# Kernel tuning notes

Measured on AMD Instinct MI355X. Metric: run time of the kernel, lower is better.

Reference implementation:

```python
import jax, jax.numpy as jnp
import numpy as np

B, N, M, C, H = 2, 2048, 512, 1536, 12
HD = C // H          # 128 head dim
RD = 64              # partial rotary dim (rotary_dim in torch code)
EPS = 1e-6


def setup_inputs() -> dict:
    key = jax.random.key(0)
    ks = jax.random.split(key, 8)
    x = jax.random.normal(ks[0], (B, N, C), dtype=jnp.float32)
    y = jax.random.normal(ks[1], (B, M, C), dtype=jnp.float32)
    # realistic rope table: pos[n, j, 0]=cos, pos[n, j, 1]=sin, j over RD//2 freqs
    t = jnp.arange(N, dtype=jnp.float32)
    inv_freq = 1.0 / (10000.0 ** (jnp.arange(RD // 2, dtype=jnp.float32) / (RD // 2)))
    ang = t[:, None] * inv_freq[None, :]                     # [N, RD/2]
    pos = jnp.stack([jnp.cos(ang), jnp.sin(ang)], axis=-1)   # [N, RD/2, 2]
    y_token_weights = jax.random.uniform(ks[2], (B, M), dtype=jnp.float32, minval=0.05, maxval=2.0)
    s = 0.02
    Wqkv = jax.random.normal(ks[3], (C, 3 * C), dtype=jnp.float32) * s
    Wkv = jax.random.normal(ks[4], (C, 2 * C), dtype=jnp.float32) * s
    q_norm_w = jnp.ones((HD,), dtype=jnp.float32)
    k_norm_w = jnp.ones((HD,), dtype=jnp.float32)
    Wproj = jax.random.normal(ks[5], (C, C), dtype=jnp.float32) * s
    bproj = jnp.zeros((C,), dtype=jnp.float32)
    return {"x": x, "y": y, "pos": pos, "y_token_weights": y_token_weights,
            "Wqkv": Wqkv, "Wkv": Wkv, "q_norm_w": q_norm_w, "k_norm_w": k_norm_w,
            "Wproj": Wproj, "bproj": bproj}


def _rms_norm(h, w):
    # RMSNorm in fp32 then cast back (matches torch Norm)
    hf = h.astype(jnp.float32)
    var = jnp.mean(hf * hf, axis=-1, keepdims=True)
    return (w * (hf * jax.lax.rsqrt(var + EPS))).astype(h.dtype)


def _rope(q, k, pos):
    # q,k: [B,H,N,HD]; pos: [N, RD/2, 2]; rotate first RD dims only
    cos = pos[..., 0][None, None]            # [1,1,N,RD/2]
    sin = pos[..., 1][None, None]
    half = RD // 2

    def rot(t):
        t1 = t[..., :half]
        t2 = t[..., half:RD]
        t_rot = jnp.concatenate([t1 * cos - t2 * sin, t1 * sin + t2 * cos], axis=-1)
        return jnp.concatenate([t_rot, t[..., RD:]], axis=-1)

    return rot(q), rot(k)


def reference(x, y, pos, y_token_weights, Wqkv, Wkv, q_norm_w, k_norm_w, Wproj, bproj):
    # self QKV: [B,N,3C] -> [3,B,H,N,HD]
    qkv = jnp.einsum('bnc,cd->bnd', x, Wqkv).reshape(B, N, 3, H, HD).transpose(2, 0, 3, 1, 4)
    q, kx, vx = qkv[0], qkv[1], qkv[2]
    q = _rms_norm(q, q_norm_w)
    kx = _rms_norm(kx, k_norm_w)
    q, kx = _rope(q, kx, pos)

    # cross KV from y: [B,M,2C] -> [2,B,H,M,HD]
    kv = jnp.einsum('bmc,cd->bmd', y, Wkv).reshape(B, M, 2, H, HD).transpose(2, 0, 3, 1, 4)
    ky = _rms_norm(kv[0], k_norm_w)
    vy = kv[1]
    k = jnp.concatenate([kx, ky], axis=2)    # [B,H,N+M,HD]
    v = jnp.concatenate([vx, vy], axis=2)

    # additive bias: zeros over x tokens, log(clamp(w)) over y tokens
    y_bias = jnp.log(jnp.clip(y_token_weights, 1e-4, None))           # [B,M]
    attn_bias = jnp.concatenate([jnp.zeros((B, N), x.dtype), y_bias], axis=1)[:, None, None, :]

    scale = HD ** -0.5
    scores = jnp.einsum('bhnd,bhsd->bhns', q, k) * scale + attn_bias  # [B,H,N,N+M]
    attn = jax.nn.softmax(scores, axis=-1)
    out = jnp.einsum('bhns,bhsd->bhnd', attn, v)                      # [B,H,N,HD]
    out = out.transpose(0, 2, 1, 3).reshape(B, N, C)
    return jnp.einsum('bnc,cd->bnd', out, Wproj) + bproj
```

## Files before the change

kernel.cpp:

```cpp
#include <hip/hip_runtime.h>

typedef unsigned short u16;
typedef short bf16x8 __attribute__((ext_vector_type(8)));
typedef float f32x4 __attribute__((ext_vector_type(4)));
typedef u16 u16x4 __attribute__((ext_vector_type(4)));

#define DEVFN static __device__ __forceinline__

constexpr int Bz = 2, Nn = 2048, Mm = 512, Cc = 1536, Hh = 12, HD = 128;
constexpr int Ss = Nn + Mm;
constexpr float EPSV = 1e-6f;
constexpr float SCL = 0.08838834764831845f;

DEVFN u16 f2bf(float f) {
  union { float f; unsigned u; } v; v.f = f;
  unsigned r = v.u + 0x7fffu + ((v.u >> 16) & 1u);
  return (u16)(r >> 16);
}

DEVFN unsigned cvtpk(float lo, float hi) {
  unsigned r;
  asm("v_cvt_pk_bf16_f32 %0, %1, %2" : "=v"(r) : "v"(lo), "v"(hi));
  return r;
}

DEVFN void gload16(const void* g, void* l) {
  __builtin_amdgcn_global_load_lds((const __attribute__((address_space(1))) void*)g,
                                   (__attribute__((address_space(3))) void*)l, 16, 0, 0);
}

DEVFN f32x4 mfma16(bf16x8 a, bf16x8 b, f32x4 c) {
  return __builtin_amdgcn_mfma_f32_16x16x32_bf16(a, b, c, 0, 0, 0);
}


__global__ void k_convert(const float* __restrict__ in, u16* __restrict__ out, int n) {
  int i = (blockIdx.x * blockDim.x + threadIdx.x) * 4;
  if (i < n) {
    float4 v = *(const float4*)(in + i);
    u16x4 o = { f2bf(v.x), f2bf(v.y), f2bf(v.z), f2bf(v.w) };
    *(u16x4*)(out + i) = o;
  }
}

__global__ void k_transpose_conv(const float* __restrict__ in, u16* __restrict__ out,
                                 int R, int Ccols) {
  __shared__ float t[32][33];
  int c0 = blockIdx.x * 32, r0 = blockIdx.y * 32;
  int lr = threadIdx.x >> 5, lc = threadIdx.x & 31;
#pragma unroll
  for (int i = 0; i < 4; ++i)
    t[lr + 8 * i][lc] = in[(long)(r0 + lr + 8 * i) * Ccols + c0 + lc];
  __syncthreads();
#pragma unroll
  for (int i = 0; i < 4; ++i)
    out[(long)(c0 + lr + 8 * i) * R + r0 + lc] = f2bf(t[lc][lr + 8 * i]);
}

__global__ void k_bias(const float* __restrict__ w, float* __restrict__ bias) {
  int i = blockIdx.x * 256 + threadIdx.x;
  if (i < Bz * Ss) {
    int b = i / Ss, s = i % Ss;
    bias[i] = (s < Nn) ? 0.0f : logf(fmaxf(w[b * Mm + s - Nn], 1e-4f));
  }
}

template <int MODE>
__global__ __launch_bounds__(256, 2) void k_gemm(
    const u16* __restrict__ A, const u16* __restrict__ Bt,
    int K, int NC, int rowsPerB,
    const float* __restrict__ pos, const float* __restrict__ qnw,
    const float* __restrict__ knw, const float* __restrict__ bprj,
    u16* __restrict__ qout, u16* __restrict__ kout, u16* __restrict__ vout,
    float* __restrict__ fout) {
  __shared__ __align__(16) u16 As[2][128 * 64];
  __shared__ __align__(16) u16 Bs[2][128 * 64];
  __shared__ float red[256];
  const int tid = threadIdx.x;
  const int lane = tid & 63;
  const int wid = tid >> 6;
  const int g = lane >> 4, cl = lane & 15;
  const int wr = wid >> 1, wc = wid & 1;
  const long m0 = (long)blockIdx.x * 128, n0 = (long)blockIdx.y * 128;

  f32x4 acc[4][4] = {};

  const int arow0 = tid >> 3;
  const int sxb = (((tid & 7) ^ (arow0 & 7)) << 4);
  const long K2 = (long)K * 2;
  const char* Abase = (const char*)A + (m0 + arow0) * K2 + sxb;
  const char* Bbase = (const char*)Bt + (n0 + arow0) * K2 + sxb;
  const int dtid = tid * 16;

  auto STAGE = [&](int kt, int s) {
    char* ad = (char*)As[s];
    char* bd = (char*)Bs[s];
    const long ko = (long)kt * 128;
#pragma unroll
    for (int i = 0; i < 4; ++i) {
      gload16(Abase + i * 32 * K2 + ko, ad + i * 4096 + dtid);
      gload16(Bbase + i * 32 * K2 + ko, bd + i * 4096 + dtid);
    }
  };

  const int nt = K / 64;
  STAGE(0, 0);
  int cur = 0;
  for (int kt = 0; kt < nt; ++kt) {
    __syncthreads();
    if (kt + 1 < nt) STAGE(kt + 1, cur ^ 1);
    const char* as = (const char*)As[cur];
    const char* bs = (const char*)Bs[cur];
#pragma unroll
    for (int s = 0; s < 2; ++s) {
      bf16x8 af[4], bfr[4];
#pragma unroll
      for (int m = 0; m < 4; ++m) {
        int row = wr * 64 + m * 16 + cl;
        af[m] = *(const bf16x8*)(as + row * 128 + (((s * 4 + g) ^ (row & 7)) << 4));
      }
#pragma unroll
      for (int n = 0; n < 4; ++n) {
        int row = wc * 64 + n * 16 + cl;
        bfr[n] = *(const bf16x8*)(bs + row * 128 + (((s * 4 + g) ^ (row & 7)) << 4));
      }
#pragma unroll
      for (int m = 0; m < 4; ++m)
#pragma unroll
        for (int n = 0; n < 4; ++n)
          acc[m][n] = mfma16(af[m], bfr[n], acc[m][n]);
    }
    cur ^= 1;
  }

  if (MODE == 0) {
#pragma unroll
    for (int n = 0; n < 4; ++n) {
      int col = (int)n0 + wc * 64 + n * 16 + cl;
      float bv = bprj[col];
#pragma unroll
      for (int m = 0; m < 4; ++m)
#pragma unroll
        for (int r = 0; r < 4; ++r) {
          long row = m0 + wr * 64 + m * 16 + 4 * g + r;
          fout[row * NC + col] = acc[m][n][r] + bv;
        }
    }
    return;
  }

  const int ct = blockIdx.y;
  const int s_idx = ct / Hh, h = ct % Hh;
  const int bb = (int)(m0 / rowsPerB);
  const int bh = bb * Hh + h;
  const int seq0 = (int)(m0 % rowsPerB) + wr * 64;
  const bool is_v = (MODE == 1) ? (s_idx == 2) : (s_idx == 1);
  const bool do_norm = !is_v;
  const bool do_rope = (MODE == 1) && (s_idx < 2);

  if (is_v) {
    const long s0 = (MODE == 2 ? Nn : 0) + seq0;
#pragma unroll
    for (int m = 0; m < 4; ++m) {
      long sb = s0 + m * 16 + 4 * g;
#pragma unroll
      for (int n = 0; n < 4; ++n) {
        int d = wc * 64 + n * 16 + cl;
        u16x4 pk = { f2bf(acc[m][n][0]), f2bf(acc[m][n][1]),
                     f2bf(acc[m][n][2]), f2bf(acc[m][n][3]) };
        *(u16x4*)(vout + ((long)bh * HD + d) * Ss + sb) = pk;
      }
    }
    return;
  }

  if (do_norm) {
    float rs[4][4];
#pragma unroll
    for (int m = 0; m < 4; ++m)
#pragma unroll
      for (int r = 0; r < 4; ++r) {
        float t = 0.f;
#pragma unroll
        for (int n = 0; n < 4; ++n) t += acc[m][n][r] * acc[m][n][r];
        t += __shfl_xor(t, 1);
        t += __shfl_xor(t, 2);
        t += __shfl_xor(t, 4);
        t += __shfl_xor(t, 8);
        if (cl == 0) red[wc * 128 + wr * 64 + m * 16 + 4 * g + r] = t;
      }
    __syncthreads();
#pragma unroll
    for (int m = 0; m < 4; ++m)
#pragma unroll
      for (int r = 0; r < 4; ++r) {
        int row = wr * 64 + m * 16 + 4 * g + r;
        rs[m][r] = rsqrtf((red[row] + red[128 + row]) * (1.0f / 128.0f) + EPSV);
      }
    const float* nw = (MODE == 1 && s_idx == 0) ? qnw : knw;
    const float nsc = (MODE == 1 && s_idx == 0) ? SCL : 1.0f;
#pragma unroll
    for (int n = 0; n < 4; ++n) {
      float nwv = nw[wc * 64 + n * 16 + cl] * nsc;
#pragma unroll
      for (int m = 0; m < 4; ++m)
#pragma unroll
        for (int r = 0; r < 4; ++r) acc[m][n][r] *= rs[m][r] * nwv;
    }
  }

  if (do_rope && wc == 0) {
#pragma unroll
    for (int m = 0; m < 4; ++m)
#pragma unroll
      for (int r = 0; r < 4; ++r) {
        int seq = seq0 + m * 16 + 4 * g + r;
#pragma unroll
        for (int n = 0; n < 2; ++n) {
          int d = n * 16 + cl;
          float cs = pos[(seq * 32 + d) * 2 + 0];
          float sn = pos[(seq * 32 + d) * 2 + 1];
          float t1 = acc[m][n][r], t2 = acc[m][n + 2][r];
          acc[m][n][r] = t1 * cs - t2 * sn;
          acc[m][n + 2][r] = t1 * sn + t2 * cs;
        }
      }
  }

  u16* ob;
  long sbase;
  if (MODE == 1) {
    if (s_idx == 0) { ob = qout; sbase = (long)bh * Nn; }
    else { ob = kout; sbase = (long)bh * Ss; }
  } else {
    ob = kout;
    sbase = (long)bh * Ss + Nn;
  }
#pragma unroll
  for (int m = 0; m < 4; ++m)
#pragma unroll
    for (int r = 0; r < 4; ++r) {
      long rowb = (sbase + seq0 + m * 16 + 4 * g + r) * HD;
#pragma unroll
      for (int n = 0; n < 4; ++n)
        ob[rowb + wc * 64 + n * 16 + cl] = f2bf(acc[m][n][r]);
    }
}

__global__ __launch_bounds__(256, 2) void k_flash(
    const u16* __restrict__ Q, const u16* __restrict__ K, const u16* __restrict__ Vt,
    const float* __restrict__ bias, u16* __restrict__ Aout) {
  __shared__ __align__(16) u16 Ks[2][64 * 128];
  __shared__ __align__(16) u16 Vs[2][128 * 64];
  __shared__ __align__(16) u16 Ps[4][16 * 64];
  const int tid = threadIdx.x, lane = tid & 63, wid = tid >> 6;
  const int g = lane >> 4, cl = lane & 15;
  const int bh = blockIdx.y, b = bh / Hh, h = bh % Hh;
  const int n0 = blockIdx.x * 128;
  constexpr int NT = Ss / 64;

  const u16* Qg = Q + ((long)bh * Nn + n0 + wid * 32) * HD;
  const char* Kg = (const char*)(K + (long)bh * Ss * HD);
  const char* Vg = (const char*)(Vt + (long)bh * HD * Ss);
  const float* bg = bias + b * Ss;

  bf16x8 qf[2][4];
#pragma unroll
  for (int m = 0; m < 2; ++m)
#pragma unroll
    for (int kk = 0; kk < 4; ++kk)
      qf[m][kk] = *(const bf16x8*)(Qg + (m * 16 + cl) * HD + kk * 32 + g * 8);

  const int krow = tid >> 4;
  const char* Ksrc = Kg + krow * 256 + (((tid & 15) ^ (krow & 7)) << 4);
  const int vrow = tid >> 3;
  const char* Vsrc = Vg + (long)vrow * (Ss * 2) + (((tid & 7) ^ (vrow & 7)) << 4);
  const int dsto = (tid & ~63) << 4;

  auto STAGE = [&](int t, int s) {
    char* kd = (char*)Ks[s] + dsto;
    char* vd = (char*)Vs[s] + dsto;
    long kb = (long)t * 64;
#pragma unroll
    for (int i = 0; i < 4; ++i) gload16(Ksrc + kb * 256 + i * (16 * 256), kd + i * 4096);
#pragma unroll
    for (int i = 0; i < 4; ++i) gload16(Vsrc + kb * 2 + (long)i * 32 * (Ss * 2), vd + i * 4096);
  };

  f32x4 ov[2][8] = {};
  float mi[2] = {-3e38f, -3e38f}, li[2] = {0.f, 0.f};
  u16* pt = (u16*)Ps[wid];
  const int h7 = (cl & 7) << 1;

  STAGE(0, 0);
  __syncthreads();
  int cur = 0;
  for (int t = 0; t < NT; ++t) {
    if (t + 1 < NT) STAGE(t + 1, cur ^ 1);
    const bool biased = (t * 64 >= Nn);
    float badd[4][4];
    if (biased) {
#pragma unroll
      for (int n = 0; n < 4; ++n)
#pragma unroll
        for (int r = 0; r < 4; ++r)
          badd[n][r] = bg[t * 64 + n * 16 + 4 * g + r];
    }
    const char* ks = (const char*)Ks[cur];
    const char* vs = (const char*)Vs[cur];

    f32x4 sc[2][4] = {};
#pragma unroll
    for (int n = 0; n < 4; ++n) {
      int krw = n * 16 + cl;
#pragma unroll
      for (int kk = 0; kk < 4; ++kk) {
        bf16x8 kf = *(const bf16x8*)(ks + krw * 256 + (((kk * 4 + g) ^ (krw & 7)) << 4));
        sc[0][n] = mfma16(kf, qf[0][kk], sc[0][n]);
        sc[1][n] = mfma16(kf, qf[1][kk], sc[1][n]);
      }
    }

    float co_s[2];
#pragma unroll
    for (int m = 0; m < 2; ++m) {
      float mx = -3e38f;
#pragma unroll
      for (int n = 0; n < 4; ++n)
#pragma unroll
        for (int r = 0; r < 4; ++r) {
          float s = sc[m][n][r];
          if (biased) s += badd[n][r];
          sc[m][n][r] = s;
          mx = fmaxf(mx, s);
        }
      mx = fmaxf(mx, __shfl_xor(mx, 16));
      mx = fmaxf(mx, __shfl_xor(mx, 32));
      float mnew = fmaxf(mi[m], mx);
      float co = __expf(mi[m] - mnew);
      mi[m] = mnew;
      float rsum = 0.f;
#pragma unroll
      for (int n = 0; n < 4; ++n)
#pragma unroll
        for (int r = 0; r < 4; ++r) {
          float p = __expf(sc[m][n][r] - mnew);
          sc[m][n][r] = p;
          rsum += p;
        }
      rsum += __shfl_xor(rsum, 16);
      rsum += __shfl_xor(rsum, 32);
      li[m] = li[m] * co + rsum;
      co_s[m] = co;
    }

#pragma unroll
    for (int m = 0; m < 2; ++m)
#pragma unroll
      for (int r = 0; r < 4; ++r) {
        float cr = __shfl(co_s[m], 4 * g + r, 64);
#pragma unroll
        for (int nd = 0; nd < 8; ++nd) ov[m][nd][r] *= cr;
      }

    bf16x8 pf[2][2];
#pragma unroll
    for (int m = 0; m < 2; ++m) {
#pragma unroll
      for (int n = 0; n < 4; ++n) {
        uint2 w;
        w.x = cvtpk(sc[m][n][0], sc[m][n][1]);
        w.y = cvtpk(sc[m][n][2], sc[m][n][3]);
        *(uint2*)((char*)pt + cl * 128 + (((4 * n + g) ^ h7) << 3)) = w;
      }
#pragma unroll
      for (int ks2 = 0; ks2 < 2; ++ks2)
        pf[m][ks2] = *(const bf16x8*)((const char*)pt + cl * 128 +
                                      (((8 * ks2 + 2 * g) ^ h7) << 3));
    }

#pragma unroll
    for (int nd = 0; nd < 8; ++nd) {
      int vrw = nd * 16 + cl;
#pragma unroll
      for (int ks2 = 0; ks2 < 2; ++ks2) {
        bf16x8 vf = *(const bf16x8*)(vs + vrw * 128 + (((ks2 * 4 + g) ^ (vrw & 7)) << 4));
        ov[0][nd] = mfma16(pf[0][ks2], vf, ov[0][nd]);
        ov[1][nd] = mfma16(pf[1][ks2], vf, ov[1][nd]);
      }
    }
    __syncthreads();
    cur ^= 1;
  }

#pragma unroll
  for (int m = 0; m < 2; ++m) {
    float inv = 1.0f / li[m];
#pragma unroll
    for (int r = 0; r < 4; ++r) {
      float iv = __shfl(inv, 4 * g + r, 64);
      long row = (long)b * Nn + n0 + wid * 32 + m * 16 + 4 * g + r;
      long base = row * Cc + h * HD;
#pragma unroll
      for (int nd = 0; nd < 8; ++nd)
        Aout[base + nd * 16 + cl] = f2bf(ov[m][nd][r] * iv);
    }
  }
}


extern "C" void kernel_launch(void* const* d_in, const int* in_sizes, int n_in,
                              void* d_out, int out_size, void* d_ws, size_t ws_size,
                              hipStream_t stream) {
  const float* x = (const float*)d_in[0];
  const float* y = (const float*)d_in[1];
  const float* pos = (const float*)d_in[2];
  const float* ytw = (const float*)d_in[3];
  const float* Wqkv = (const float*)d_in[4];
  const float* Wkv = (const float*)d_in[5];
  const float* qnw = (const float*)d_in[6];
  const float* knw = (const float*)d_in[7];
  const float* Wproj = (const float*)d_in[8];
  const float* bproj = (const float*)d_in[9];
  float* out = (float*)d_out;
  char* ws = (char*)d_ws;

  size_t o = 0;
  auto take = [&](size_t b) {
    char* p = ws + o;
    o += (b + 255) & ~(size_t)255;
    return p;
  };
  u16* xb = (u16*)take((size_t)Bz * Nn * Cc * 2);
  u16* yb = (u16*)take((size_t)Bz * Mm * Cc * 2);
  u16* wqkvt = (u16*)take((size_t)3 * Cc * Cc * 2);
  u16* wkvt = (u16*)take((size_t)2 * Cc * Cc * 2);
  u16* wprjt = (u16*)take((size_t)Cc * Cc * 2);
  u16* qb = (u16*)take((size_t)Bz * Hh * Nn * HD * 2);
  u16* kb = (u16*)take((size_t)Bz * Hh * Ss * HD * 2);
  u16* vtb = (u16*)take((size_t)Bz * Hh * Ss * HD * 2);
  u16* ab = (u16*)take((size_t)Bz * Nn * Cc * 2);
  float* bias = (float*)take((size_t)Bz * Ss * 4);

  k_convert<<<dim3(Bz * Nn * Cc / 1024), 256, 0, stream>>>(x, xb, Bz * Nn * Cc);
  k_convert<<<dim3(Bz * Mm * Cc / 1024), 256, 0, stream>>>(y, yb, Bz * Mm * Cc);
  k_transpose_conv<<<dim3(3 * Cc / 32, Cc / 32), 256, 0, stream>>>(Wqkv, wqkvt, Cc, 3 * Cc);
  k_transpose_conv<<<dim3(2 * Cc / 32, Cc / 32), 256, 0, stream>>>(Wkv, wkvt, Cc, 2 * Cc);
  k_transpose_conv<<<dim3(Cc / 32, Cc / 32), 256, 0, stream>>>(Wproj, wprjt, Cc, Cc);
  k_bias<<<dim3((Bz * Ss + 255) / 256), 256, 0, stream>>>(ytw, bias);
  k_gemm<1><<<dim3(Bz * Nn / 128, 3 * Cc / 128), 256, 0, stream>>>(
      xb, wqkvt, Cc, 3 * Cc, Nn, pos, qnw, knw, nullptr, qb, kb, vtb, nullptr);
  k_gemm<2><<<dim3(Bz * Mm / 128, 2 * Cc / 128), 256, 0, stream>>>(
      yb, wkvt, Cc, 2 * Cc, Mm, pos, qnw, knw, nullptr, nullptr, kb, vtb, nullptr);
  k_flash<<<dim3(Nn / 128, Bz * Hh), 256, 0, stream>>>(qb, kb, vtb, bias, ab);
  k_gemm<0><<<dim3(Bz * Nn / 128, Cc / 128), 256, 0, stream>>>(
      ab, wprjt, Cc, Cc, Nn, nullptr, nullptr, nullptr, bproj, nullptr, nullptr, nullptr, out);
}
```

Baseline: 411.4 us.

## Single-buffer GEMM for occupancy, add XCD swizzle, setprio, and lazy softmax rescale

The GEMM drops LDS double buffering in favour of a single buffer with two barriers per k-step, and raises launch bounds to 3-4 waves per SIMD to gain occupancy. Both the GEMM and flash kernels remap block IDs with an XCD-aware swizzle so neighbouring tiles land on the same chiplet's L2. MFMA sections are wrapped in s_setprio. The flash softmax skips rescaling the output accumulator unless the running max grows by more than 8, which trades a small amount of exponent headroom for fewer multiplies. Losing the prefetch overlap in the GEMM risks exposing load latency.

Result: faster. 401.5 us (-2.4%).

```diff
diff --git a/kernel.cpp b/kernel.cpp
--- a/kernel.cpp
+++ b/kernel.cpp
@@ -31,6 +31,11 @@
 
 DEVFN f32x4 mfma16(bf16x8 a, bf16x8 b, f32x4 c) {
   return __builtin_amdgcn_mfma_f32_16x16x32_bf16(a, b, c, 0, 0, 0);
+}
+
+DEVFN int xcdswz(int hw, int nwg) {
+  int q = nwg >> 3;
+  return (hw & 7) * q + (hw >> 3);
 }
 
 
@@ -66,22 +71,27 @@
 }
 
 template <int MODE>
-__global__ __launch_bounds__(256, 2) void k_gemm(
+__global__ __launch_bounds__(256, MODE == 0 ? 4 : 3) void k_gemm(
     const u16* __restrict__ A, const u16* __restrict__ Bt,
     int K, int NC, int rowsPerB,
     const float* __restrict__ pos, const float* __restrict__ qnw,
     const float* __restrict__ knw, const float* __restrict__ bprj,
     u16* __restrict__ qout, u16* __restrict__ kout, u16* __restrict__ vout,
     float* __restrict__ fout) {
-  __shared__ __align__(16) u16 As[2][128 * 64];
-  __shared__ __align__(16) u16 Bs[2][128 * 64];
+  __shared__ __align__(16) u16 As[128 * 64];
+  __shared__ __align__(16) u16 Bs[128 * 64];
   __shared__ float red[256];
   const int tid = threadIdx.x;
   const int lane = tid & 63;
   const int wid = tid >> 6;
   const int g = lane >> 4, cl = lane & 15;
   const int wr = wid >> 1, wc = wid & 1;
-  const long m0 = (long)blockIdx.x * 128, n0 = (long)blockIdx.y * 128;
+
+  const int gx = gridDim.x;
+  const int hw = blockIdx.x + gx * blockIdx.y;
+  const int wg = xcdswz(hw, gx * gridDim.y);
+  const int bx = wg % gx, by = wg / gx;
+  const long m0 = (long)bx * 128, n0 = (long)by * 128;
 
   f32x4 acc[4][4] = {};
 
@@ -92,37 +102,29 @@
   const char* Bbase = (const char*)Bt + (n0 + arow0) * K2 + sxb;
   const int dtid = tid * 16;
 
-  auto STAGE = [&](int kt, int s) {
-    char* ad = (char*)As[s];
-    char* bd = (char*)Bs[s];
-    const long ko = (long)kt * 128;
-#pragma unroll
-    for (int i = 0; i < 4; ++i) {
-      gload16(Abase + i * 32 * K2 + ko, ad + i * 4096 + dtid);
-      gload16(Bbase + i * 32 * K2 + ko, bd + i * 4096 + dtid);
-    }
-  };
-
   const int nt = K / 64;
-  STAGE(0, 0);
-  int cur = 0;
   for (int kt = 0; kt < nt; ++kt) {
     __syncthreads();
-    if (kt + 1 < nt) STAGE(kt + 1, cur ^ 1);
-    const char* as = (const char*)As[cur];
-    const char* bs = (const char*)Bs[cur];
+    const long ko = (long)kt * 128;
+#pragma unroll
+    for (int i = 0; i < 4; ++i) {
+      gload16(Abase + i * 32 * K2 + ko, (char*)As + i * 4096 + dtid);
+      gload16(Bbase + i * 32 * K2 + ko, (char*)Bs + i * 4096 + dtid);
+    }
+    __syncthreads();
+    __builtin_amdgcn_s_setprio(1);
 #pragma unroll
     for (int s = 0; s < 2; ++s) {
       bf16x8 af[4], bfr[4];
 #pragma unroll
       for (int m = 0; m < 4; ++m) {
         int row = wr * 64 + m * 16 + cl;
-        af[m] = *(const bf16x8*)(as + row * 128 + (((s * 4 + g) ^ (row & 7)) << 4));
+        af[m] = *(const bf16x8*)((const char*)As + row * 128 + (((s * 4 + g) ^ (row & 7)) << 4));
       }
 #pragma unroll
       for (int n = 0; n < 4; ++n) {
         int row = wc * 64 + n * 16 + cl;
-        bfr[n] = *(const bf16x8*)(bs + row * 128 + (((s * 4 + g) ^ (row & 7)) << 4));
+        bfr[n] = *(const bf16x8*)((const char*)Bs + row * 128 + (((s * 4 + g) ^ (row & 7)) << 4));
       }
 #pragma unroll
       for (int m = 0; m < 4; ++m)
@@ -130,7 +132,7 @@
         for (int n = 0; n < 4; ++n)
           acc[m][n] = mfma16(af[m], bfr[n], acc[m][n]);
     }
-    cur ^= 1;
+    __builtin_amdgcn_s_setprio(0);
   }
 
   if (MODE == 0) {
@@ -149,7 +151,7 @@
     return;
   }
 
-  const int ct = blockIdx.y;
+  const int ct = by;
   const int s_idx = ct / Hh, h = ct % Hh;
   const int bb = (int)(m0 / rowsPerB);
   const int bh = bb * Hh + h;
@@ -255,8 +257,11 @@
   __shared__ __align__(16) u16 Ps[4][16 * 64];
   const int tid = threadIdx.x, lane = tid & 63, wid = tid >> 6;
   const int g = lane >> 4, cl = lane & 15;
-  const int bh = blockIdx.y, b = bh / Hh, h = bh % Hh;
-  const int n0 = blockIdx.x * 128;
+  const int hw = blockIdx.x + gridDim.x * blockIdx.y;
+  const int wg = xcdswz(hw, gridDim.x * gridDim.y);
+  const int qt = wg % gridDim.x, bh = wg / gridDim.x;
+  const int b = bh / Hh, h = bh % Hh;
+  const int n0 = qt * 128;
   constexpr int NT = Ss / 64;
 
   const u16* Qg = Q + ((long)bh * Nn + n0 + wid * 32) * HD;
@@ -310,6 +315,7 @@
     const char* vs = (const char*)Vs[cur];
 
     f32x4 sc[2][4] = {};
+    __builtin_amdgcn_s_setprio(1);
 #pragma unroll
     for (int n = 0; n < 4; ++n) {
       int krw = n * 16 + cl;
@@ -320,8 +326,9 @@
         sc[1][n] = mfma16(kf, qf[1][kk], sc[1][n]);
       }
     }
-
-    float co_s[2];
+    __builtin_amdgcn_s_setprio(0);
+
+    float pmax[2];
 #pragma unroll
     for (int m = 0; m < 2; ++m) {
       float mx = -3e38f;
@@ -336,32 +343,41 @@
         }
       mx = fmaxf(mx, __shfl_xor(mx, 16));
       mx = fmaxf(mx, __shfl_xor(mx, 32));
-      float mnew = fmaxf(mi[m], mx);
-      float co = __expf(mi[m] - mnew);
-      mi[m] = mnew;
+      pmax[m] = mx;
+    }
+    if (__any((pmax[0] > mi[0] + 8.f) || (pmax[1] > mi[1] + 8.f))) {
+      float co_s[2];
+#pragma unroll
+      for (int m = 0; m < 2; ++m) {
+        float mnew = fmaxf(mi[m], pmax[m]);
+        co_s[m] = __expf(mi[m] - mnew);
+        mi[m] = mnew;
+        li[m] *= co_s[m];
+      }
+#pragma unroll
+      for (int m = 0; m < 2; ++m)
+#pragma unroll
+        for (int r = 0; r < 4; ++r) {
+          float cr = __shfl(co_s[m], 4 * g + r, 64);
+#pragma unroll
+          for (int nd = 0; nd < 8; ++nd) ov[m][nd][r] *= cr;
+        }
+    }
+#pragma unroll
+    for (int m = 0; m < 2; ++m) {
       float rsum = 0.f;
 #pragma unroll
       for (int n = 0; n < 4; ++n)
 #pragma unroll
         for (int r = 0; r < 4; ++r) {
-          float p = __expf(sc[m][n][r] - mnew);
+          float p = __expf(sc[m][n][r] - mi[m]);
           sc[m][n][r] = p;
           rsum += p;
         }
       rsum += __shfl_xor(rsum, 16);
       rsum += __shfl_xor(rsum, 32);
-      li[m] = li[m] * co + rsum;
-      co_s[m] = co;
-    }
-
-#pragma unroll
-    for (int m = 0; m < 2; ++m)
-#pragma unroll
-      for (int r = 0; r < 4; ++r) {
-        float cr = __shfl(co_s[m], 4 * g + r, 64);
-#pragma unroll
-        for (int nd = 0; nd < 8; ++nd) ov[m][nd][r] *= cr;
-      }
+      li[m] += rsum;
+    }
 
     bf16x8 pf[2][2];
 #pragma unroll
@@ -379,6 +395,7 @@
                                       (((8 * ks2 + 2 * g) ^ h7) << 3));
     }
 
+    __builtin_amdgcn_s_setprio(1);
 #pragma unroll
     for (int nd = 0; nd < 8; ++nd) {
       int vrw = nd * 16 + cl;
@@ -389,6 +406,7 @@
         ov[1][nd] = mfma16(pf[1][ks2], vf, ov[1][nd]);
       }
     }
+    __builtin_amdgcn_s_setprio(0);
     __syncthreads();
     cur ^= 1;
   }
```
